# Kernel tuning notes

Measured on AMD Instinct MI355X. Metric: run time of the kernel, lower is better.

The kernel has to match this reference:

```python
import jax, jax.numpy as jnp
import numpy as np

EMBED = 1024
HEADS = 16
HEAD_DIM = EMBED // HEADS
N, L = 2, 2048


def setup_inputs() -> dict:
    key = jax.random.key(0)
    ks = jax.random.split(key, 9)
    s = 0.02
    return {
        "values": jax.random.normal(ks[0], (N, L, EMBED), jnp.float32),
        "key": jax.random.normal(ks[1], (N, L, EMBED), jnp.float32),
        "query": jax.random.normal(ks[2], (N, L, EMBED), jnp.float32),
        "mask": jnp.ones((N, 1, 1, L), jnp.int32),
        "Wv": jax.random.normal(ks[3], (HEAD_DIM, HEAD_DIM), jnp.float32) * s,
        "Wk": jax.random.normal(ks[4], (HEAD_DIM, HEAD_DIM), jnp.float32) * s,
        "Wq": jax.random.normal(ks[5], (HEAD_DIM, HEAD_DIM), jnp.float32) * s,
        "bq": jax.random.normal(ks[6], (HEAD_DIM,), jnp.float32) * s,
        "Wo": jax.random.normal(ks[7], (EMBED, EMBED), jnp.float32) * s,
        "bo": jax.random.normal(ks[8], (EMBED,), jnp.float32) * s,
    }


def reference(values, key, query, mask, Wv, Wk, Wq, bq, Wo, bo):
    n, q_len, E = query.shape
    D = Wv.shape[0]
    H = E // D
    # split heads: (N, len, H, D)
    v = values.reshape(n, -1, H, D)
    k = key.reshape(n, -1, H, D)
    q = query.reshape(n, q_len, H, D)
    # per-head linear projections (torch Linear: x @ W.T [+ b])
    v = jnp.einsum("nlhd,ed->nlhe", v, Wv)
    k = jnp.einsum("nlhd,ed->nlhe", k, Wk)
    q = jnp.einsum("nlhd,ed->nlhe", q, Wq) + bq
    # scores: (N, H, q_len, k_len)
    energy = jnp.einsum("nqhd,nkhd->nhqk", q, k)
    energy = jnp.where(mask == 0, jnp.float32(-1e20), energy)
    # NOTE: original scales by sqrt(embed_size), not sqrt(head_dim)
    attn = jax.nn.softmax(energy / jnp.sqrt(jnp.float32(E)), axis=-1)
    out = jnp.einsum("nhqk,nkhd->nqhd", attn, v).reshape(n, q_len, E)
    return out @ Wo.T + bo
```

## Files before the change

kernel.cpp:

```cpp
#include <hip/hip_runtime.h>
#include <hip/hip_bf16.h>
#include <string.h>

#define NB   2
#define SEQ  2048
#define EMB  1024
#define NH   16
#define HD   64
#define QSCALE 0.045084219f
#define MADD2  -4.5084219e18f

typedef __attribute__((ext_vector_type(8))) short short8;
typedef __attribute__((ext_vector_type(4))) float f32x4;

#define MFMA(a, b, c) __builtin_amdgcn_mfma_f32_16x16x32_bf16(a, b, c, 0, 0, 0)
#define EXP2(x) __builtin_amdgcn_exp2f(x)

__device__ __forceinline__ unsigned short f2bf(float x) {
    union { float f; unsigned u; } v; v.f = x;
    unsigned r = v.u + 0x7fffu + ((v.u >> 16) & 1u);
    return (unsigned short)(r >> 16);
}
__device__ __forceinline__ unsigned packbf2(float a, float b) {
    __hip_bfloat162 h = __float22bfloat162_rn(make_float2(a, b));
    unsigned u; memcpy(&u, &h, 4);
    return u;
}

__global__ __launch_bounds__(256) void cvt_kernel(
    const float* __restrict__ Wo, const float* __restrict__ Wq,
    const float* __restrict__ Wk, const float* __restrict__ Wv,
    const int* __restrict__ mask,
    unsigned short* __restrict__ Wob, unsigned short* __restrict__ Wqb,
    unsigned short* __restrict__ Wkb, unsigned short* __restrict__ Wvb,
    float* __restrict__ maddG)
{
    const int b = blockIdx.x, tid = threadIdx.x;
    if (b < 1024) {
        int idx = b * 256 + tid;
        float4 w = ((const float4*)Wo)[idx];
        uint2 p; p.x = packbf2(w.x, w.y); p.y = packbf2(w.z, w.w);
        ((uint2*)Wob)[idx] = p;
    } else if (b < 1027) {
        const float* W = (b == 1024) ? Wq : (b == 1025) ? Wk : Wv;
        unsigned short* Wb = (b == 1024) ? Wqb : (b == 1025) ? Wkb : Wvb;
        #pragma unroll
        for (int i = 0; i < 4; ++i) {
            int idx = tid + i * 256;
            float4 w = ((const float4*)W)[idx];
            uint2 p; p.x = packbf2(w.x, w.y); p.y = packbf2(w.z, w.w);
            ((uint2*)Wb)[idx] = p;
        }
    } else {
        #pragma unroll
        for (int i = 0; i < 16; ++i) {
            int idx = tid + i * 256;
            maddG[idx] = mask[idx] ? 0.f : MADD2;
        }
    }
}

__global__ __launch_bounds__(256) void qkv_kernel(
    const float* __restrict__ Qin, const float* __restrict__ Kin,
    const float* __restrict__ Vin,
    const unsigned short* __restrict__ Wqb, const unsigned short* __restrict__ Wkb,
    const unsigned short* __restrict__ Wvb, const float* __restrict__ bq,
    unsigned short* __restrict__ Qp, unsigned short* __restrict__ Kp,
    unsigned short* __restrict__ Vtp)
{
    const int lt = blockIdx.x;
    const int h  = blockIdx.y;
    const int tz = blockIdx.z;
    const int t  = tz >> 1, n = tz & 1;

    const float* X; const unsigned short* Wb;
    if (t == 0)      { X = Qin; Wb = Wqb; }
    else if (t == 1) { X = Kin; Wb = Wkb; }
    else             { X = Vin; Wb = Wvb; }

    __shared__ __align__(16) unsigned short sX[128][70];
    __shared__ __align__(16) unsigned short sT[64][136];

    const int tid = threadIdx.x, wave = tid >> 6, lane = tid & 63;
    const int ln = lane & 15, quad = lane >> 4;

    #pragma unroll
    for (int i = 0; i < 8; ++i) {
        int flat = tid + i * 256;
        int r = flat >> 4, c4 = flat & 15;
        float4 xv = *(const float4*)(X + ((size_t)(n * SEQ + lt * 128 + r)) * EMB + h * HD + c4 * 4);
        uint2 xp; xp.x = packbf2(xv.x, xv.y); xp.y = packbf2(xv.z, xv.w);
        *(uint2*)&sX[r][c4 * 4] = xp;
    }
    short8 wf0[4], wf1[4];
    #pragma unroll
    for (int nt = 0; nt < 4; ++nt) {
        wf0[nt] = *(const short8*)(Wb + (nt * 16 + ln) * HD + quad * 8);
        wf1[nt] = *(const short8*)(Wb + (nt * 16 + ln) * HD + 32 + quad * 8);
    }
    __syncthreads();

    f32x4 acc[2][4];
    #pragma unroll
    for (int set = 0; set < 2; ++set) {
        short8 af0 = *(const short8*)&sX[wave * 32 + set * 16 + ln][quad * 8];
        short8 af1 = *(const short8*)&sX[wave * 32 + set * 16 + ln][32 + quad * 8];
        #pragma unroll
        for (int nt = 0; nt < 4; ++nt) {
            f32x4 a = {0.f, 0.f, 0.f, 0.f};
            a = MFMA(af0, wf0[nt], a);
            a = MFMA(af1, wf1[nt], a);
            acc[set][nt] = a;
        }
    }

    if (t == 0) {
        #pragma unroll
        for (int nt = 0; nt < 4; ++nt) {
            float bb = bq[nt * 16 + ln];
            #pragma unroll
            for (int set = 0; set < 2; ++set)
                #pragma unroll
                for (int a = 0; a < 4; ++a)
                    acc[set][nt][a] = (acc[set][nt][a] + bb) * QSCALE;
        }
    }

    if (t < 2) {
        unsigned short* Out = (t == 0) ? Qp : Kp;
        #pragma unroll
        for (int set = 0; set < 2; ++set)
            #pragma unroll
            for (int a = 0; a < 4; ++a) {
                size_t row = (size_t)((n * NH + h) * SEQ + lt * 128 + wave * 32 + set * 16 + quad * 4 + a);
                #pragma unroll
                for (int nt = 0; nt < 4; ++nt)
                    Out[row * HD + nt * 16 + ln] = f2bf(acc[set][nt][a]);
            }
    } else {
        #pragma unroll
        for (int set = 0; set < 2; ++set)
            #pragma unroll
            for (int nt = 0; nt < 4; ++nt)
                #pragma unroll
                for (int a = 0; a < 4; ++a)
                    sT[nt * 16 + ln][wave * 32 + set * 16 + quad * 4 + a] = f2bf(acc[set][nt][a]);
        __syncthreads();
        #pragma unroll
        for (int i = 0; i < 4; ++i) {
            int flat = tid + i * 256;
            int r = flat >> 4, c8 = flat & 15;
            *(float4*)(Vtp + ((size_t)((n * NH + h) * HD + r)) * SEQ + lt * 128 + c8 * 8) =
                *(const float4*)&sT[r][c8 * 8];
        }
    }
}

__global__ __launch_bounds__(128, 2) void flash_kernel(
    const unsigned short* __restrict__ Qp, const unsigned short* __restrict__ Kp,
    const unsigned short* __restrict__ Vtp, const float* __restrict__ maddG,
    unsigned short* __restrict__ A )
{
    const int nh = blockIdx.x;
    const int qt = blockIdx.y;
    const int n  = nh >> 4, h = nh & 15;

    const int tid  = threadIdx.x;
    const int wave = tid >> 6, lane = tid & 63;
    const int ln   = lane & 15, quad = lane >> 4;

    __shared__ __align__(16) unsigned short sP[2][64][72];
    float (*xO)[65] = reinterpret_cast<float(*)[65]>(&sP[0][0][0]);
    float* xl = reinterpret_cast<float*>(reinterpret_cast<char*>(&sP[0][0][0]) + 64 * 65 * 4);

    const unsigned short* Qb = Qp + ((size_t)nh * SEQ + qt * 64) * HD;
    short8 qf[4][2];
    #pragma unroll
    for (int set = 0; set < 4; ++set) {
        qf[set][0] = *(const short8*)(Qb + (set * 16 + ln) * HD + quad * 8);
        qf[set][1] = *(const short8*)(Qb + (set * 16 + ln) * HD + 32 + quad * 8);
    }

    const unsigned short* Kb = Kp  + (size_t)nh * SEQ * HD;
    const unsigned short* Vb = Vtp + (size_t)nh * HD * SEQ;
    const float* mb = maddG + n * SEQ;

    f32x4 o[4][4];
    #pragma unroll
    for (int s2 = 0; s2 < 4; ++s2)
        #pragma unroll
        for (int dt = 0; dt < 4; ++dt) o[s2][dt] = (f32x4){0.f, 0.f, 0.f, 0.f};
    float lsum[4] = {0.f, 0.f, 0.f, 0.f};

    const int kt0 = wave * (SEQ / 64 / 2);
    for (int kt = kt0; kt < kt0 + SEQ / 64 / 2; ++kt) {
        short8 vf[4][2];
        #pragma unroll
        for (int dt = 0; dt < 4; ++dt) {
            const unsigned short* vr = Vb + (size_t)(dt * 16 + ln) * SEQ + kt * 64;
            vf[dt][0] = *(const short8*)(vr + quad * 8);
            vf[dt][1] = *(const short8*)(vr + 32 + quad * 8);
        }

        #pragma unroll
        for (int nt = 0; nt < 4; ++nt) {
            const unsigned short* kr = Kb + (size_t)(kt * 64 + nt * 16 + ln) * HD;
            short8 kf0 = *(const short8*)(kr + quad * 8);
            short8 kf1 = *(const short8*)(kr + 32 + quad * 8);
            float4 md  = *(const float4*)(mb + kt * 64 + nt * 16 + quad * 4);

            #pragma unroll
            for (int set = 0; set < 4; ++set) {
                f32x4 z = {0.f, 0.f, 0.f, 0.f};
                z = MFMA(kf0, qf[set][0], z);
                z = MFMA(kf1, qf[set][1], z);
                float p0 = EXP2(fminf(z[0] + md.x, 80.f));
                float p1 = EXP2(fminf(z[1] + md.y, 80.f));
                float p2 = EXP2(fminf(z[2] + md.z, 80.f));
                float p3 = EXP2(fminf(z[3] + md.w, 80.f));
                lsum[set] += (p0 + p1) + (p2 + p3);
                uint2 w; w.x = packbf2(p0, p1); w.y = packbf2(p2, p3);
                *(uint2*)&sP[wave][set * 16 + ln][nt * 16 + quad * 4] = w;
            }
        }
        asm volatile("s_waitcnt lgkmcnt(0)" ::: "memory");

        #pragma unroll
        for (int set = 0; set < 4; ++set) {
            short8 pf0 = *(const short8*)&sP[wave][set * 16 + ln][quad * 8];
            short8 pf1 = *(const short8*)&sP[wave][set * 16 + ln][32 + quad * 8];
            #pragma unroll
            for (int dt = 0; dt < 4; ++dt) {
                o[set][dt] = MFMA(pf0, vf[dt][0], o[set][dt]);
                o[set][dt] = MFMA(pf1, vf[dt][1], o[set][dt]);
            }
        }
    }

    float lf[4];
    #pragma unroll
    for (int set = 0; set < 4; ++set) {
        float l = lsum[set];
        l += __shfl_xor(l, 16);
        l += __shfl_xor(l, 32);
        lf[set] = l;
    }

    __syncthreads();
    if (wave == 1) {
        #pragma unroll
        for (int set = 0; set < 4; ++set) {
            #pragma unroll
            for (int a = 0; a < 4; ++a)
                #pragma unroll
                for (int dt = 0; dt < 4; ++dt)
                    xO[set * 16 + quad * 4 + a][dt * 16 + ln] = o[set][dt][a];
            if (quad == 0) xl[set * 16 + ln] = lf[set];
        }
    }
    __syncthreads();
    if (wave == 0) {
        #pragma unroll
        for (int set = 0; set < 4; ++set)
            #pragma unroll
            for (int a = 0; a < 4; ++a) {
                int q = set * 16 + quad * 4 + a;
                float l0 = __shfl(lf[set], q & 15);
                float inv = 1.0f / (l0 + xl[q]);
                size_t row = (size_t)(n * SEQ + qt * 64 + q);
                #pragma unroll
                for (int dt = 0; dt < 4; ++dt)
                    A[row * EMB + h * HD + dt * 16 + ln] =
                        f2bf((o[set][dt][a] + xO[q][dt * 16 + ln]) * inv);
            }
    }
}

__global__ __launch_bounds__(256) void outproj_kernel(
    const unsigned short* __restrict__ A, const unsigned short* __restrict__ Wob,
    const float* __restrict__ bo, float* __restrict__ Out)
{
    const int ct = blockIdx.x;
    const int rt = blockIdx.y;

    const int tid  = threadIdx.x;
    const int wave = tid >> 6, lane = tid & 63;
    const int ln   = lane & 15, quad = lane >> 4;
    const int wm   = wave >> 1, wn = wave & 1;

    __shared__ __align__(16) unsigned short sA[128][72];
    __shared__ __align__(16) unsigned short sB[128][72];

    f32x4 acc[4][4];
    #pragma unroll
    for (int i = 0; i < 4; ++i)
        #pragma unroll
        for (int j = 0; j < 4; ++j) acc[i][j] = (f32x4){0.f, 0.f, 0.f, 0.f};

    for (int kc = 0; kc < EMB / 64; ++kc) {
        __syncthreads();
        #pragma unroll
        for (int i = 0; i < 4; ++i) {
            int flat = tid + i * 256;
            int r = flat >> 3, c8 = flat & 7;
            *(float4*)&sA[r][c8 * 8] =
                *(const float4*)(A + (size_t)(rt * 128 + r) * EMB + kc * 64 + c8 * 8);
            *(float4*)&sB[r][c8 * 8] =
                *(const float4*)(Wob + (size_t)(ct * 128 + r) * EMB + kc * 64 + c8 * 8);
        }
        __syncthreads();

        #pragma unroll
        for (int ks = 0; ks < 2; ++ks) {
            short8 af[4], bf[4];
            #pragma unroll
            for (int i = 0; i < 4; ++i)
                af[i] = *(const short8*)&sA[wm * 64 + i * 16 + ln][ks * 32 + quad * 8];
            #pragma unroll
            for (int j = 0; j < 4; ++j)
                bf[j] = *(const short8*)&sB[wn * 64 + j * 16 + ln][ks * 32 + quad * 8];
            #pragma unroll
            for (int i = 0; i < 4; ++i)
                #pragma unroll
                for (int j = 0; j < 4; ++j)
                    acc[i][j] = MFMA(af[i], bf[j], acc[i][j]);
        }
    }

    #pragma unroll
    for (int j = 0; j < 4; ++j) {
        int col = ct * 128 + wn * 64 + j * 16 + ln;
        float bb = bo[col];
        #pragma unroll
        for (int i = 0; i < 4; ++i)
            #pragma unroll
            for (int a = 0; a < 4; ++a) {
                size_t row = (size_t)(rt * 128 + wm * 64 + i * 16 + quad * 4 + a);
                Out[row * EMB + col] = acc[i][j][a] + bb;
            }
    }
}

extern "C" void kernel_launch(void* const* d_in, const int* in_sizes, int n_in,
                              void* d_out, int out_size, void* d_ws, size_t ws_size,
                              hipStream_t stream) {
    const float* values = (const float*)d_in[0];
    const float* key_   = (const float*)d_in[1];
    const float* query  = (const float*)d_in[2];
    const int*   mask   = (const int*)d_in[3];
    const float* Wv     = (const float*)d_in[4];
    const float* Wk     = (const float*)d_in[5];
    const float* Wq     = (const float*)d_in[6];
    const float* bq     = (const float*)d_in[7];
    const float* Wo     = (const float*)d_in[8];
    const float* bo     = (const float*)d_in[9];
    float* out = (float*)d_out;

    const size_t NHLD = (size_t)NB * NH * SEQ * HD;

    unsigned short* ws = (unsigned short*)d_ws;
    unsigned short* Qp    = ws;
    unsigned short* Kp    = ws + NHLD;
    unsigned short* Vtp   = ws + 2 * NHLD;
    unsigned short* Aattn = ws + 3 * NHLD;
    unsigned short* Wob   = ws + 4 * NHLD;
    unsigned short* Wqb   = Wob + (size_t)EMB * EMB;
    unsigned short* Wkb   = Wqb + HD * HD;
    unsigned short* Wvb   = Wkb + HD * HD;
    float* maddG = (float*)(Wvb + HD * HD);

    cvt_kernel<<<dim3(1028), 256, 0, stream>>>(
        Wo, Wq, Wk, Wv, mask, Wob, Wqb, Wkb, Wvb, maddG);
    qkv_kernel<<<dim3(SEQ / 128, NH, 3 * NB), 256, 0, stream>>>(
        query, key_, values, Wqb, Wkb, Wvb, bq, Qp, Kp, Vtp);
    flash_kernel<<<dim3(NB * NH, SEQ / 64), 128, 0, stream>>>(
        Qp, Kp, Vtp, maddG, Aattn);
    outproj_kernel<<<dim3(EMB / 128, NB * SEQ / 128), 256, 0, stream>>>(
        Aattn, Wob, bo, out);
}
```

Baseline: 210.6 us.

## Split flash keys across four waves and drop LDS staging in output projection

The flash kernel now runs four waves per block, each handling a quarter of the key range, and merges the partial outputs and row sums through a tree reduction in shared memory. The exp2 clamp is removed. The output projection is rewritten so that each wave independently computes a 64x64 tile, loading operands straight from global memory with no LDS staging and no block barriers. This trades per-wave parallelism and fewer syncs against more reduction overhead, more redundant global loads in the GEMM, and the loss of overflow protection in the exponent.

```diff
diff --git a/kernel.cpp b/kernel.cpp
--- a/kernel.cpp
+++ b/kernel.cpp
@@ -156,7 +156,7 @@
     }
 }
 
-__global__ __launch_bounds__(128, 2) void flash_kernel(
+__global__ __launch_bounds__(256, 4) void flash_kernel(
     const unsigned short* __restrict__ Qp, const unsigned short* __restrict__ Kp,
     const unsigned short* __restrict__ Vtp, const float* __restrict__ maddG,
     unsigned short* __restrict__ A )
@@ -169,9 +169,11 @@
     const int wave = tid >> 6, lane = tid & 63;
     const int ln   = lane & 15, quad = lane >> 4;
 
-    __shared__ __align__(16) unsigned short sP[2][64][72];
-    float (*xO)[65] = reinterpret_cast<float(*)[65]>(&sP[0][0][0]);
-    float* xl = reinterpret_cast<float*>(reinterpret_cast<char*>(&sP[0][0][0]) + 64 * 65 * 4);
+    __shared__ __align__(16) unsigned short sP[4][64][72];
+    __shared__ float xl[4][64];
+    float (*xO0)[66] = reinterpret_cast<float(*)[66]>(&sP[0][0][0]);
+    float (*xO1)[66] = reinterpret_cast<float(*)[66]>(
+        reinterpret_cast<char*>(&sP[0][0][0]) + 64 * 66 * 4);
 
     const unsigned short* Qb = Qp + ((size_t)nh * SEQ + qt * 64) * HD;
     short8 qf[4][2];
@@ -192,8 +194,8 @@
         for (int dt = 0; dt < 4; ++dt) o[s2][dt] = (f32x4){0.f, 0.f, 0.f, 0.f};
     float lsum[4] = {0.f, 0.f, 0.f, 0.f};
 
-    const int kt0 = wave * (SEQ / 64 / 2);
-    for (int kt = kt0; kt < kt0 + SEQ / 64 / 2; ++kt) {
+    const int kt0 = wave * (SEQ / 64 / 4);
+    for (int kt = kt0; kt < kt0 + SEQ / 64 / 4; ++kt) {
         short8 vf[4][2];
         #pragma unroll
         for (int dt = 0; dt < 4; ++dt) {
@@ -214,10 +216,10 @@
                 f32x4 z = {0.f, 0.f, 0.f, 0.f};
                 z = MFMA(kf0, qf[set][0], z);
                 z = MFMA(kf1, qf[set][1], z);
-                float p0 = EXP2(fminf(z[0] + md.x, 80.f));
-                float p1 = EXP2(fminf(z[1] + md.y, 80.f));
-                float p2 = EXP2(fminf(z[2] + md.z, 80.f));
-                float p3 = EXP2(fminf(z[3] + md.w, 80.f));
+                float p0 = EXP2(z[0] + md.x);
+                float p1 = EXP2(z[1] + md.y);
+                float p2 = EXP2(z[2] + md.z);
+                float p3 = EXP2(z[3] + md.w);
                 lsum[set] += (p0 + p1) + (p2 + p3);
                 uint2 w; w.x = packbf2(p0, p1); w.y = packbf2(p2, p3);
                 *(uint2*)&sP[wave][set * 16 + ln][nt * 16 + quad * 4] = w;
@@ -245,34 +247,60 @@
         l += __shfl_xor(l, 32);
         lf[set] = l;
     }
-
-    __syncthreads();
-    if (wave == 1) {
-        #pragma unroll
-        for (int set = 0; set < 4; ++set) {
+    if (quad == 0) {
+        #pragma unroll
+        for (int set = 0; set < 4; ++set) xl[wave][set * 16 + ln] = lf[set];
+    }
+
+    __syncthreads();
+    if (wave & 1) {
+        float (*xO)[66] = (wave == 1) ? xO0 : xO1;
+        #pragma unroll
+        for (int set = 0; set < 4; ++set)
             #pragma unroll
             for (int a = 0; a < 4; ++a)
                 #pragma unroll
                 for (int dt = 0; dt < 4; ++dt)
                     xO[set * 16 + quad * 4 + a][dt * 16 + ln] = o[set][dt][a];
-            if (quad == 0) xl[set * 16 + ln] = lf[set];
-        }
+    }
+    __syncthreads();
+    if (!(wave & 1)) {
+        float (*xO)[66] = (wave == 0) ? xO0 : xO1;
+        #pragma unroll
+        for (int set = 0; set < 4; ++set)
+            #pragma unroll
+            for (int a = 0; a < 4; ++a)
+                #pragma unroll
+                for (int dt = 0; dt < 4; ++dt)
+                    o[set][dt][a] += xO[set * 16 + quad * 4 + a][dt * 16 + ln];
+    }
+    __syncthreads();
+    if (wave == 2) {
+        #pragma unroll
+        for (int set = 0; set < 4; ++set)
+            #pragma unroll
+            for (int a = 0; a < 4; ++a)
+                #pragma unroll
+                for (int dt = 0; dt < 4; ++dt)
+                    xO0[set * 16 + quad * 4 + a][dt * 16 + ln] = o[set][dt][a];
     }
     __syncthreads();
     if (wave == 0) {
         #pragma unroll
-        for (int set = 0; set < 4; ++set)
+        for (int set = 0; set < 4; ++set) {
+            float lfull = xl[0][set * 16 + ln] + xl[1][set * 16 + ln] +
+                          xl[2][set * 16 + ln] + xl[3][set * 16 + ln];
             #pragma unroll
             for (int a = 0; a < 4; ++a) {
                 int q = set * 16 + quad * 4 + a;
-                float l0 = __shfl(lf[set], q & 15);
-                float inv = 1.0f / (l0 + xl[q]);
+                float inv = 1.0f / __shfl(lfull, quad * 4 + a);
                 size_t row = (size_t)(n * SEQ + qt * 64 + q);
                 #pragma unroll
                 for (int dt = 0; dt < 4; ++dt)
                     A[row * EMB + h * HD + dt * 16 + ln] =
-                        f2bf((o[set][dt][a] + xO[q][dt * 16 + ln]) * inv);
-            }
+                        f2bf((o[set][dt][a] + xO0[q][dt * 16 + ln]) * inv);
+            }
+        }
     }
 }
 
@@ -280,16 +308,13 @@
     const unsigned short* __restrict__ A, const unsigned short* __restrict__ Wob,
     const float* __restrict__ bo, float* __restrict__ Out)
 {
-    const int ct = blockIdx.x;
-    const int rt = blockIdx.y;
-
-    const int tid  = threadIdx.x;
-    const int wave = tid >> 6, lane = tid & 63;
-    const int ln   = lane & 15, quad = lane >> 4;
-    const int wm   = wave >> 1, wn = wave & 1;
-
-    __shared__ __align__(16) unsigned short sA[128][72];
-    __shared__ __align__(16) unsigned short sB[128][72];
+    const int tid = threadIdx.x, wave = tid >> 6, lane = tid & 63;
+    const int ln = lane & 15, quad = lane >> 4;
+    const int id = blockIdx.x * 4 + wave;
+    const int mt = id >> 4, nt4 = id & 15;
+
+    const unsigned short* Ab = A   + (size_t)(mt * 64) * EMB;
+    const unsigned short* Bb = Wob + (size_t)(nt4 * 64) * EMB;
 
     f32x4 acc[4][4];
     #pragma unroll
@@ -297,45 +322,30 @@
         #pragma unroll
         for (int j = 0; j < 4; ++j) acc[i][j] = (f32x4){0.f, 0.f, 0.f, 0.f};
 
-    for (int kc = 0; kc < EMB / 64; ++kc) {
-        __syncthreads();
-        #pragma unroll
-        for (int i = 0; i < 4; ++i) {
-            int flat = tid + i * 256;
-            int r = flat >> 3, c8 = flat & 7;
-            *(float4*)&sA[r][c8 * 8] =
-                *(const float4*)(A + (size_t)(rt * 128 + r) * EMB + kc * 64 + c8 * 8);
-            *(float4*)&sB[r][c8 * 8] =
-                *(const float4*)(Wob + (size_t)(ct * 128 + r) * EMB + kc * 64 + c8 * 8);
-        }
-        __syncthreads();
-
-        #pragma unroll
-        for (int ks = 0; ks < 2; ++ks) {
-            short8 af[4], bf[4];
-            #pragma unroll
-            for (int i = 0; i < 4; ++i)
-                af[i] = *(const short8*)&sA[wm * 64 + i * 16 + ln][ks * 32 + quad * 8];
+    for (int ks = 0; ks < EMB / 32; ++ks) {
+        short8 af[4], bf[4];
+        #pragma unroll
+        for (int i = 0; i < 4; ++i)
+            af[i] = *(const short8*)(Ab + (size_t)(i * 16 + ln) * EMB + ks * 32 + quad * 8);
+        #pragma unroll
+        for (int j = 0; j < 4; ++j)
+            bf[j] = *(const short8*)(Bb + (size_t)(j * 16 + ln) * EMB + ks * 32 + quad * 8);
+        #pragma unroll
+        for (int i = 0; i < 4; ++i)
             #pragma unroll
             for (int j = 0; j < 4; ++j)
-                bf[j] = *(const short8*)&sB[wn * 64 + j * 16 + ln][ks * 32 + quad * 8];
-            #pragma unroll
-            for (int i = 0; i < 4; ++i)
-                #pragma unroll
-                for (int j = 0; j < 4; ++j)
-                    acc[i][j] = MFMA(af[i], bf[j], acc[i][j]);
-        }
+                acc[i][j] = MFMA(af[i], bf[j], acc[i][j]);
     }
 
     #pragma unroll
     for (int j = 0; j < 4; ++j) {
-        int col = ct * 128 + wn * 64 + j * 16 + ln;
+        int col = nt4 * 64 + j * 16 + ln;
         float bb = bo[col];
         #pragma unroll
         for (int i = 0; i < 4; ++i)
             #pragma unroll
             for (int a = 0; a < 4; ++a) {
-                size_t row = (size_t)(rt * 128 + wm * 64 + i * 16 + quad * 4 + a);
+                size_t row = (size_t)(mt * 64 + i * 16 + quad * 4 + a);
                 Out[row * EMB + col] = acc[i][j][a] + bb;
             }
     }
@@ -373,8 +383,8 @@
         Wo, Wq, Wk, Wv, mask, Wob, Wqb, Wkb, Wvb, maddG);
     qkv_kernel<<<dim3(SEQ / 128, NH, 3 * NB), 256, 0, stream>>>(
         query, key_, values, Wqb, Wkb, Wvb, bq, Qp, Kp, Vtp);
-    flash_kernel<<<dim3(NB * NH, SEQ / 64), 128, 0, stream>>>(
+    flash_kernel<<<dim3(NB * NH, SEQ / 64), 256, 0, stream>>>(
         Qp, Kp, Vtp, maddG, Aattn);
-    outproj_kernel<<<dim3(EMB / 128, NB * SEQ / 128), 256, 0, stream>>>(
+    outproj_kernel<<<dim3(256), 256, 0, stream>>>(
         Aattn, Wob, bo, out);
 }
```

Measured after the change: 503.8 us. +139.2%, slower.
